# Kernel optimization log

Hardware: AMD Instinct MI355X
Metric: run time of the kernel (lower is better)

Reference implementation:

```python
import jax, jax.numpy as jnp
import numpy as np

B, IC, N = 32, 1, 64
KN, KS, PAD = 128, 65, 16
R, LAT = 8, 32
LEAK = 0.01
THETA_PRIOR = float(np.pi)
HW = N + 2 * PAD - KS + 1  # 32
OFFSETS = np.array([0, np.pi/4, np.pi/2, 3*np.pi/4, np.pi, -3*np.pi/4, -np.pi/2, -np.pi/4], dtype=np.float32)


def rotate_filters(w, n_rot):
    """Bilinear rotation of [O,I,k,k] filters for n_rot angles, matching
    F.affine_grid/F.grid_sample with align_corners=False, zero padding.
    Returns [O*n_rot, I, k, k] (rotation-major within each O block)."""
    O, I, k, _ = w.shape
    thetas = (2.0 * jnp.pi / n_rot) * jnp.arange(n_rot, dtype=jnp.float32)
    coords = (2.0 * jnp.arange(k, dtype=jnp.float32) + 1.0) / k - 1.0  # normalized, align_corners=False
    yy, xx = jnp.meshgrid(coords, coords, indexing='ij')  # [k,k]
    cos = jnp.cos(thetas)[:, None, None]
    sin = jnp.sin(thetas)[:, None, None]
    xs = cos * xx + sin * yy   # [R,k,k] sample x (normalized)
    ys = -sin * xx + cos * yy  # [R,k,k] sample y
    px = ((xs + 1.0) * k - 1.0) * 0.5  # pixel coords
    py = ((ys + 1.0) * k - 1.0) * 0.5
    x0 = jnp.floor(px); y0 = jnp.floor(py)
    wx = px - x0; wy = py - y0

    def gather(yi, xi):
        valid = (yi >= 0) & (yi < k) & (xi >= 0) & (xi < k)
        yc = jnp.clip(yi, 0, k - 1).astype(jnp.int32)
        xc = jnp.clip(xi, 0, k - 1).astype(jnp.int32)
        v = w[:, :, yc, xc]  # [O,I,R,k,k]
        return v * valid.astype(w.dtype)

    out = (gather(y0, x0) * (1 - wy) * (1 - wx)
           + gather(y0, x0 + 1) * (1 - wy) * wx
           + gather(y0 + 1, x0) * wy * (1 - wx)
           + gather(y0 + 1, x0 + 1) * wy * wx)  # [O,I,R,k,k]
    return jnp.transpose(out, (0, 2, 1, 3, 4)).reshape(O * n_rot, I, k, k)


def conv1x1(h, w, b):
    # h: [B,C,R,H,W], w: [O,C], b: [O] -- Conv3d with 1x1x1 kernel
    return jnp.einsum('bcrhw,oc->borhw', h, w) + b[None, :, None, None, None]


def _forward(x, w1, b1, w2, b2, wa, ba, wr, br, wz, bz, gumbel):
    tw = rotate_filters(w1[:, :, 0], R)  # [KN*R, IC, KS, KS]
    y = jax.lax.conv_general_dilated(
        x, tw, window_strides=(1, 1), padding=[(PAD, PAD), (PAD, PAD)],
        dimension_numbers=('NCHW', 'OIHW', 'NCHW'))
    Bn = y.shape[0]
    y = y.reshape(Bn, KN, R, HW, HW) + b1[None, :, None, None, None]
    xa = jax.nn.leaky_relu(y, LEAK)
    h = jax.nn.leaky_relu(conv1x1(xa, w2, b2), LEAK)
    attn = conv1x1(h, wa, ba)[:, 0]  # [B,R,H,W]
    offsets = jnp.asarray(OFFSETS)
    # Normal(0, theta_prior).log_prob(offsets)
    p_r = (-0.5 * (offsets / THETA_PRIOR) ** 2
           - jnp.log(THETA_PRIOR) - 0.5 * jnp.log(2.0 * jnp.pi))[:, None, None]  # [R,1,1]
    attn = attn + p_r  # broadcast over batch
    flat = attn.reshape(Bn, -1)
    q_t_r = jax.nn.log_softmax(flat, axis=1).reshape(attn.shape)
    a_sampled = jax.nn.softmax(flat + gumbel.reshape(Bn, -1), axis=-1).reshape(Bn, R, HW, HW)
    z = conv1x1(h, wz, bz)      # [B,2*LAT,R,H,W]
    theta = conv1x1(h, wr, br)  # [B,2,R,H,W]
    theta_mu = theta[:, 0] + offsets[None, :, None, None]
    theta = jnp.stack((theta_mu, theta[:, 1]), axis=1)
    return attn, q_t_r, p_r, a_sampled, offsets, theta, z


def setup_inputs():
    key = jax.random.key(0)
    ks = jax.random.split(key, 12)
    stdv1 = 1.0 / np.sqrt(IC * KS * KS)
    stdv2 = 1.0 / np.sqrt(KN)
    def unif(k, shape, a):
        return jax.random.uniform(k, shape, jnp.float32, -a, a)
    u = jax.random.uniform(ks[11], (B, R, HW, HW), jnp.float32, 1e-6, 1.0 - 1e-6)
    gumbel = -jnp.log(-jnp.log(u))
    return {
        'x': jax.random.normal(ks[0], (B, IC, N, N), jnp.float32),
        'w1': unif(ks[1], (KN, IC, 1, KS, KS), stdv1),
        'b1': unif(ks[2], (KN,), stdv1),
        'w2': unif(ks[3], (KN, KN), stdv2),
        'b2': unif(ks[4], (KN,), stdv2),
        'wa': unif(ks[5], (1, KN), stdv2),
        'ba': unif(ks[6], (1,), stdv2),
        'wr': unif(ks[7], (2, KN), stdv2),
        'br': unif(ks[8], (2,), stdv2),
        'wz': unif(ks[9], (2 * LAT, KN), stdv2),
        'bz': unif(ks[10], (2 * LAT,), stdv2),
        'gumbel': gumbel,
    }


def reference(x, w1, b1, w2, b2, wa, ba, wr, br, wz, bz, gumbel):
    return _forward(x, w1, b1, w2, b2, wa, ba, wr, br, wz, bz, gumbel)
```

## Files before the change

### kernel.cpp

```cpp
#include <hip/hip_runtime.h>
#include <hip/hip_bf16.h>

typedef unsigned int u32;
typedef unsigned short u16;

#define KYP 72
#define KPAD 4736
#define NK   74

#define OUT_ATTN 0
#define OUT_QTR  262144
#define OUT_PR   524288
#define OUT_AS   524296
#define OUT_OFF  786440
#define OUT_TH   786448
#define OUT_Z    1310736

typedef __attribute__((ext_vector_type(8))) short bf16x8;
typedef __attribute__((ext_vector_type(4))) float f32x4;

__device__ const float OFFS[8] = {
  0.0f,
  0.78539816339744830961f,
  1.57079632679489661923f,
  2.35619449019234492885f,
  3.14159265358979323846f,
 -2.35619449019234492885f,
 -1.57079632679489661923f,
 -0.78539816339744830961f
};

__device__ __forceinline__ float leaky_(float v){ return v >= 0.0f ? v : 0.01f*v; }

__device__ __forceinline__ u16 f2bf(float f){
  u32 x = __float_as_uint(f);
  u32 r = (x + 0x7FFFu + ((x >> 16) & 1u)) >> 16;
  return (u16)r;
}

__device__ __forceinline__ void gload_lds16(const void* g, void* l){
  __builtin_amdgcn_global_load_lds((const __attribute__((address_space(1))) u32*)g,
                                   (__attribute__((address_space(3))) u32*)l, 16, 0, 0);
}

#define BARRIER() { asm volatile("" ::: "memory"); __builtin_amdgcn_s_barrier(); asm volatile("" ::: "memory"); }
#define WAITV(N)  asm volatile("s_waitcnt vmcnt(" #N ")" ::: "memory")
#define LGK0()    { asm volatile("s_waitcnt lgkmcnt(0)" ::: "memory"); __builtin_amdgcn_sched_barrier(0); }
#define SCHEDB()  __builtin_amdgcn_sched_barrier(0)

__global__ __launch_bounds__(256) void xshift_kernel(const float* __restrict__ x, u16* __restrict__ xsh){
  int t = blockIdx.x*256 + threadIdx.x;
  if (t >= 393216) return;
  int c8  = t & 15;
  int u   = t >> 4;
  int row = u % 96;
  int v   = u / 96;
  int b   = v & 31;
  int s   = v >> 5;
  int iy = row - 16;
  u16 h[8];
#pragma unroll
  for (int j = 0; j < 8; ++j){
    int ix = c8*8 + j + s - 16;
    float val = 0.0f;
    if (iy >= 0 && iy < 64 && ix >= 0 && ix < 64) val = x[(b*64 + iy)*64 + ix];
    h[j] = f2bf(val);
  }
  uint4 pk;
  pk.x = (u32)h[0] | ((u32)h[1] << 16);
  pk.y = (u32)h[2] | ((u32)h[3] << 16);
  pk.z = (u32)h[4] | ((u32)h[5] << 16);
  pk.w = (u32)h[6] | ((u32)h[7] << 16);
  ((uint4*)xsh)[t] = pk;
}

__global__ __launch_bounds__(256) void rotate_kernel(const float* __restrict__ w1, u16* __restrict__ twb){
  __shared__ float wsh[4225];
  int n = blockIdx.x;
  int kn = n & 127, rot = n >> 7;
  for (int i = threadIdx.x; i < 4225; i += 256) wsh[i] = w1[kn*4225 + i];
  __syncthreads();
  float th  = 0.78539816339744830961f * (float)rot;
  float cth = cosf(th), sth = sinf(th);
  for (int t = threadIdx.x; t < KPAD; t += 256){
    int ky = t / KYP, kx = t - ky*KYP;
    u16 out = 0;
    if (ky < 65 && kx < 65){
      float yy = (2.0f*(float)ky + 1.0f)/65.0f - 1.0f;
      float xx = (2.0f*(float)kx + 1.0f)/65.0f - 1.0f;
      float xs  =  cth*xx + sth*yy;
      float ysv = -sth*xx + cth*yy;
      float px = ((xs  + 1.0f)*65.0f - 1.0f)*0.5f;
      float py = ((ysv + 1.0f)*65.0f - 1.0f)*0.5f;
      float x0 = floorf(px), y0 = floorf(py);
      float wx = px - x0, wy = py - y0;
      auto samp = [&](float yf, float xf)->float{
        bool valid = (yf >= 0.0f) && (yf < 65.0f) && (xf >= 0.0f) && (xf < 65.0f);
        int yc = (int)fminf(fmaxf(yf, 0.0f), 64.0f);
        int xc = (int)fminf(fmaxf(xf, 0.0f), 64.0f);
        return valid ? wsh[yc*65 + xc] : 0.0f;
      };
      float val = samp(y0,      x0     )*(1.0f-wy)*(1.0f-wx)
                + samp(y0,      x0+1.0f)*(1.0f-wy)*wx
                + samp(y0+1.0f, x0     )*wy*(1.0f-wx)
                + samp(y0+1.0f, x0+1.0f)*wy*wx;
      out = f2bf(val);
    }
    twb[(size_t)n*KPAD + t] = out;
  }
}

__global__ __launch_bounds__(512, 2) void gemm_kernel(const u16* __restrict__ xsh,
                                                      const u16* __restrict__ twb,
                                                      u16* __restrict__ ys){
  __shared__ u16 AsB[2*16384];
  __shared__ u16 BsB[2*16384];

  const int bid  = blockIdx.x;
  const int nblk = bid & 3, mblk = bid >> 2;
  const int t    = threadIdx.x;
  const int lane = t & 63, w = t >> 6;
  const int wr   = w >> 2, wn = w & 3;
  const int hi8  = (lane >> 4) << 3;

  const int sr  = t >> 3;
  const int j0e = (t & 7) * 8;
  const int jsw = j0e ^ ((sr & 7) << 3);
  const int bg  = mblk >> 4;
  const int ox2 = (mblk & 15) * 2;
  int aOff[4];
#pragma unroll
  for (int c = 0; c < 4; ++c){
    int i  = c*64 + sr;
    int ox = ox2 + (i >> 7);
    int s_ = ox & 7, colb = ox & ~7;
    int b_ = (bg << 2) + ((i & 127) >> 5);
    int oy = i & 31;
    aOff[c] = ((s_*32 + b_)*96 + oy)*128 + colb;
  }
  const u16* bPtr[4];
#pragma unroll
  for (int c = 0; c < 4; ++c){
    int nloc = c*64 + sr;
    bPtr[c] = twb + (size_t)(nblk*256 + nloc)*KPAD + jsw;
  }

  auto stageA4 = [&](int kt, u16* dstbase){
    int k = kt*64 + jsw;
    u32 ky = (u32)k / (u32)KYP;
    int kx0 = k - (int)ky*KYP;
    bool pad = (ky >= 65);
    int kofs = (int)ky*128 + kx0;
    const int ord[4] = {0, 2, 1, 3};
#pragma unroll
    for (int ii = 0; ii < 4; ++ii){
      int c = ord[ii];
      int gofs = pad ? 0 : (aOff[c] + kofs);
      gload_lds16(xsh + gofs, dstbase + c*4096 + w*512);
    }
  };
  auto stageB4 = [&](int kt, u16* dstbase){
    int ktc = (kt < NK) ? kt : (NK-1);
#pragma unroll
    for (int c = 0; c < 4; ++c)
      gload_lds16(bPtr[c] + ktc*64, dstbase + c*4096 + w*512);
  };

  f32x4 acc[8][4];
#pragma unroll
  for (int i = 0; i < 8; ++i)
#pragma unroll
    for (int j = 0; j < 4; ++j) acc[i][j] = (f32x4){0.f,0.f,0.f,0.f};
  bf16x8 amat[4][2], bmat[4][2];

  auto readA = [&](int mh, const char* Ab){
#pragma unroll
    for (int mj = 0; mj < 4; ++mj){
      int row = wr*128 + mh*64 + mj*16 + (lane & 15);
#pragma unroll
      for (int kk = 0; kk < 2; ++kk){
        int off = (row*128 + (kk*32 + hi8)*2) ^ ((row & 7) << 4);
        amat[mj][kk] = *(const bf16x8*)(Ab + off);
      }
    }
  };
  auto readB = [&](int nh, const char* Bb){
#pragma unroll
    for (int jn = 0; jn < 2; ++jn){
      int row = wn*64 + (nh*2 + jn)*16 + (lane & 15);
#pragma unroll
      for (int kk = 0; kk < 2; ++kk){
        int off = (row*128 + (kk*32 + hi8)*2) ^ ((row & 7) << 4);
        bmat[nh*2 + jn][kk] = *(const bf16x8*)(Bb + off);
      }
    }
  };
  auto mfma16 = [&](int MH, int NH){
    __builtin_amdgcn_s_setprio(1);
#pragma unroll
    for (int mj = 0; mj < 4; ++mj)
#pragma unroll
      for (int jn = 0; jn < 2; ++jn)
#pragma unroll
        for (int kk = 0; kk < 2; ++kk)
          acc[MH*4+mj][NH*2+jn] = __builtin_amdgcn_mfma_f32_16x16x32_bf16(
              amat[mj][kk], bmat[NH*2+jn][kk], acc[MH*4+mj][NH*2+jn], 0, 0, 0);
    __builtin_amdgcn_s_setprio(0);
  };

  u16* const A0 = AsB;
  u16* const B0 = BsB;
  u16* const A1 = AsB + 16384;
  u16* const B1 = BsB + 16384;

  stageB4(0, B0);
  stageA4(0, A0);
  WAITV(2);
  BARRIER();

  for (int kt = 0; kt < NK; ++kt){
    u16* Ab = (kt & 1) ? A1 : A0;
    u16* Bb = (kt & 1) ? B1 : B0;
    u16* An = (kt & 1) ? A0 : A1;
    u16* Bn = (kt & 1) ? B0 : B1;
    readA(0, (const char*)Ab); readB(0, (const char*)Bb);
    stageB4(kt+1, Bn);
    BARRIER();
    LGK0();
    mfma16(0, 0);
    SCHEDB();
    BARRIER();
    readB(1, (const char*)Bb);
    stageA4(kt+1, An);
    BARRIER();
    LGK0();
    mfma16(0, 1);
    SCHEDB();
    WAITV(8);
    BARRIER();
    readA(1, (const char*)Ab);
    BARRIER();
    LGK0();
    mfma16(1, 1);
    SCHEDB();
    BARRIER();
    mfma16(1, 0);
    SCHEDB();
    WAITV(2);
    BARRIER();
  }

  const int m_base = mblk*256 + wr*128;
  const int n_base = nblk*256 + wn*64;
  const int rsub = (lane >> 4) << 2;
  const int csub = lane & 15;
#pragma unroll
  for (int mf = 0; mf < 8; ++mf)
#pragma unroll
    for (int nf = 0; nf < 4; ++nf)
#pragma unroll
      for (int j = 0; j < 4; ++j){
        int m = m_base + mf*16 + rsub + j;
        int n = n_base + nf*16 + csub;
        ys[(size_t)m*1024 + n] = f2bf(acc[mf][nf][j]);
      }
}

__global__ __launch_bounds__(512) void mix_kernel(const u16* __restrict__ ys,
    const float* __restrict__ b1, const float* __restrict__ w2, const float* __restrict__ b2,
    const float* __restrict__ wa, const float* __restrict__ ba,
    const float* __restrict__ wr, const float* __restrict__ br,
    const float* __restrict__ wz, const float* __restrict__ bz,
    float* __restrict__ out){
  __shared__ __align__(16) u16 Ah[256*128];
  __shared__ __align__(16) u16 W2s[128*128];
  __shared__ __align__(16) u16 Wcs[80*128];
  __shared__ float b2s[128];
  __shared__ float bcs[80];

  const int blk = blockIdx.x;
  const int b   = blk >> 5, oy = blk & 31;
  const int t    = threadIdx.x;
  const int lane = t & 63;
  const int w    = t >> 6;

  {
    const int kn0 = (t & 15)*8;
    const int r_  = (t >> 4) & 7;
    float b1v[8];
#pragma unroll
    for (int j = 0; j < 8; ++j) b1v[j] = b1[kn0 + j];
#pragma unroll
    for (int i = 0; i < 8; ++i){
      int m_loc = 4*i + (t >> 7);
      int row_m = (((b >> 2)*32 + m_loc)*128) + (b & 3)*32 + oy;
      uint4 v = *(const uint4*)(ys + (size_t)row_m*1024 + r_*128 + kn0);
      u32 vv[4] = {v.x, v.y, v.z, v.w};
      u16 hh[8];
#pragma unroll
      for (int j = 0; j < 4; ++j){
        float lo = __uint_as_float(vv[j] << 16);
        float hi = __uint_as_float(vv[j] & 0xFFFF0000u);
        hh[2*j]   = f2bf(leaky_(lo + b1v[2*j]));
        hh[2*j+1] = f2bf(leaky_(hi + b1v[2*j+1]));
      }
      int Arow = r_*32 + m_loc;
      int off = (Arow*256 + kn0*2) ^ ((Arow & 7) << 4);
      uint4 pk;
      pk.x = (u32)hh[0] | ((u32)hh[1] << 16);
      pk.y = (u32)hh[2] | ((u32)hh[3] << 16);
      pk.z = (u32)hh[4] | ((u32)hh[5] << 16);
      pk.w = (u32)hh[6] | ((u32)hh[7] << 16);
      *(uint4*)((char*)Ah + off) = pk;
    }
  }
#pragma unroll
  for (int i = 0; i < 4; ++i){
    int ch = i*512 + t;
    int row = ch >> 4, kn0 = (ch & 15)*8;
    const float* src = w2 + row*128 + kn0;
    u16 hh[8];
#pragma unroll
    for (int j = 0; j < 8; ++j) hh[j] = f2bf(src[j]);
    int off = (row*256 + kn0*2) ^ ((row & 7) << 4);
    uint4 pk;
    pk.x = (u32)hh[0] | ((u32)hh[1] << 16);
    pk.y = (u32)hh[2] | ((u32)hh[3] << 16);
    pk.z = (u32)hh[4] | ((u32)hh[5] << 16);
    pk.w = (u32)hh[6] | ((u32)hh[7] << 16);
    *(uint4*)((char*)W2s + off) = pk;
  }
#pragma unroll
  for (int i = 0; i < 3; ++i){
    int ch = i*512 + t;
    if (ch < 1280){
      int row = ch >> 4, kn0 = (ch & 15)*8;
      const float* src = nullptr;
      if (row < 64)      src = wz + row*128 + kn0;
      else if (row == 64) src = wa + kn0;
      else if (row == 65) src = wr + kn0;
      else if (row == 66) src = wr + 128 + kn0;
      u16 hh[8];
#pragma unroll
      for (int j = 0; j < 8; ++j) hh[j] = src ? f2bf(src[j]) : (u16)0;
      int off = (row*256 + kn0*2) ^ ((row & 7) << 4);
      uint4 pk;
      pk.x = (u32)hh[0] | ((u32)hh[1] << 16);
      pk.y = (u32)hh[2] | ((u32)hh[3] << 16);
      pk.z = (u32)hh[4] | ((u32)hh[5] << 16);
      pk.w = (u32)hh[6] | ((u32)hh[7] << 16);
      *(uint4*)((char*)Wcs + off) = pk;
    }
  }
  if (t < 128) b2s[t] = b2[t];
  if (t < 80){
    float v = 0.0f;
    if (t < 64) v = bz[t];
    else if (t == 64) v = ba[0];
    else if (t == 65) v = br[0];
    else if (t == 66) v = br[1];
    bcs[t] = v;
  }
  __syncthreads();

  f32x4 acc1[2][8];
#pragma unroll
  for (int mf = 0; mf < 2; ++mf)
#pragma unroll
    for (int nf = 0; nf < 8; ++nf) acc1[mf][nf] = (f32x4){0.f,0.f,0.f,0.f};
#pragma unroll
  for (int kk = 0; kk < 128; kk += 32){
    int kb = (kk + ((lane >> 4) << 3))*2;
    bf16x8 a[2], bv[8];
#pragma unroll
    for (int mf = 0; mf < 2; ++mf){
      int row = w*32 + mf*16 + (lane & 15);
      int off = (row*256 + kb) ^ ((row & 7) << 4);
      a[mf] = *(const bf16x8*)((const char*)Ah + off);
    }
#pragma unroll
    for (int nf = 0; nf < 8; ++nf){
      int row = nf*16 + (lane & 15);
      int off = (row*256 + kb) ^ ((row & 7) << 4);
      bv[nf] = *(const bf16x8*)((const char*)W2s + off);
    }
#pragma unroll
    for (int mf = 0; mf < 2; ++mf)
#pragma unroll
      for (int nf = 0; nf < 8; ++nf)
        acc1[mf][nf] = __builtin_amdgcn_mfma_f32_16x16x32_bf16(a[mf], bv[nf], acc1[mf][nf], 0, 0, 0);
  }
  __syncthreads();

#pragma unroll
  for (int mf = 0; mf < 2; ++mf)
#pragma unroll
    for (int nf = 0; nf < 8; ++nf){
      int col = nf*16 + (lane & 15);
      float bb = b2s[col];
#pragma unroll
      for (int j = 0; j < 4; ++j){
        int row = w*32 + mf*16 + ((lane >> 4) << 2) + j;
        u16 hv = f2bf(leaky_(acc1[mf][nf][j] + bb));
        int off = (row*256 + col*2) ^ ((row & 7) << 4);
        *(u16*)((char*)Ah + off) = hv;
      }
    }
  __syncthreads();

  f32x4 acc2[2][5];
#pragma unroll
  for (int mf = 0; mf < 2; ++mf)
#pragma unroll
    for (int nf = 0; nf < 5; ++nf) acc2[mf][nf] = (f32x4){0.f,0.f,0.f,0.f};
#pragma unroll
  for (int kk = 0; kk < 128; kk += 32){
    int kb = (kk + ((lane >> 4) << 3))*2;
    bf16x8 a[2], bv[5];
#pragma unroll
    for (int mf = 0; mf < 2; ++mf){
      int row = w*32 + mf*16 + (lane & 15);
      int off = (row*256 + kb) ^ ((row & 7) << 4);
      a[mf] = *(const bf16x8*)((const char*)Ah + off);
    }
#pragma unroll
    for (int nf = 0; nf < 5; ++nf){
      int row = nf*16 + (lane & 15);
      int off = (row*256 + kb) ^ ((row & 7) << 4);
      bv[nf] = *(const bf16x8*)((const char*)Wcs + off);
    }
#pragma unroll
    for (int mf = 0; mf < 2; ++mf)
#pragma unroll
      for (int nf = 0; nf < 5; ++nf)
        acc2[mf][nf] = __builtin_amdgcn_mfma_f32_16x16x32_bf16(a[mf], bv[nf], acc2[mf][nf], 0, 0, 0);
  }

  const int r = w;
  float off_r = OFFS[r];
  float qn = off_r / 3.14159265358979323846f;
  float pr = -0.5f*qn*qn - 1.14472988584940017414f - 0.91893853320467274178f;
  const int pixb = oy*32;
#pragma unroll
  for (int mf = 0; mf < 2; ++mf)
#pragma unroll
    for (int nf = 0; nf < 5; ++nf){
      int c = nf*16 + (lane & 15);
#pragma unroll
      for (int j = 0; j < 4; ++j){
        int ox = mf*16 + ((lane >> 4) << 2) + j;
        float val = acc2[mf][nf][j];
        if (c < 64){
          out[OUT_Z + (size_t)b*524288 + (size_t)c*8192 + r*1024 + pixb + ox] = val + bcs[c];
        } else if (c == 64){
          out[OUT_ATTN + (size_t)(b*8 + r)*1024 + pixb + ox] = val + bcs[64] + pr;
        } else if (c == 65){
          out[OUT_TH + ((size_t)b*2)*8192 + r*1024 + pixb + ox] = val + bcs[65] + off_r;
        } else if (c == 66){
          out[OUT_TH + ((size_t)b*2 + 1)*8192 + r*1024 + pixb + ox] = val + bcs[66];
        }
      }
    }
}

__global__ __launch_bounds__(256) void softmax_kernel(const float* __restrict__ gumbel, float* __restrict__ out){
  __shared__ float a[8192];
  __shared__ float red[256];
  const int b = blockIdx.x, t = threadIdx.x;
  const float* attn = out + OUT_ATTN + (size_t)b*8192;
  float m = -3.0e38f;
  for (int i = t; i < 8192; i += 256){ float v = attn[i]; a[i] = v; m = fmaxf(m, v); }
  red[t] = m; __syncthreads();
#pragma unroll
  for (int s = 128; s > 0; s >>= 1){ if (t < s) red[t] = fmaxf(red[t], red[t+s]); __syncthreads(); }
  m = red[0]; __syncthreads();
  float s1 = 0.0f;
  for (int i = t; i < 8192; i += 256) s1 += expf(a[i] - m);
  red[t] = s1; __syncthreads();
#pragma unroll
  for (int s = 128; s > 0; s >>= 1){ if (t < s) red[t] += red[t+s]; __syncthreads(); }
  float lse = m + logf(red[0]);
  __syncthreads();
  float* q = out + OUT_QTR + (size_t)b*8192;
  for (int i = t; i < 8192; i += 256) q[i] = a[i] - lse;
  const float* g = gumbel + (size_t)b*8192;
  float m2 = -3.0e38f;
  for (int i = t; i < 8192; i += 256){ float v = a[i] + g[i]; a[i] = v; m2 = fmaxf(m2, v); }
  __syncthreads();
  red[t] = m2; __syncthreads();
#pragma unroll
  for (int s = 128; s > 0; s >>= 1){ if (t < s) red[t] = fmaxf(red[t], red[t+s]); __syncthreads(); }
  m2 = red[0]; __syncthreads();
  float s2 = 0.0f;
  for (int i = t; i < 8192; i += 256) s2 += expf(a[i] - m2);
  red[t] = s2; __syncthreads();
#pragma unroll
  for (int s = 128; s > 0; s >>= 1){ if (t < s) red[t] += red[t+s]; __syncthreads(); }
  float inv = 1.0f/red[0];
  float* as_ = out + OUT_AS + (size_t)b*8192;
  for (int i = t; i < 8192; i += 256) as_[i] = expf(a[i] - m2)*inv;
}

__global__ void tiny_kernel(float* __restrict__ out){
  int t = threadIdx.x;
  if (t < 8){
    float off = OFFS[t];
    out[OUT_OFF + t] = off;
    float qn = off / 3.14159265358979323846f;
    out[OUT_PR + t] = -0.5f*qn*qn - 1.14472988584940017414f - 0.91893853320467274178f;
  }
}

extern "C" void kernel_launch(void* const* d_in, const int* in_sizes, int n_in,
                              void* d_out, int out_size, void* d_ws, size_t ws_size,
                              hipStream_t stream){
  const float* x      = (const float*)d_in[0];
  const float* w1     = (const float*)d_in[1];
  const float* b1     = (const float*)d_in[2];
  const float* w2     = (const float*)d_in[3];
  const float* b2     = (const float*)d_in[4];
  const float* wa     = (const float*)d_in[5];
  const float* ba     = (const float*)d_in[6];
  const float* wr     = (const float*)d_in[7];
  const float* br     = (const float*)d_in[8];
  const float* wz     = (const float*)d_in[9];
  const float* bz     = (const float*)d_in[10];
  const float* gumbel = (const float*)d_in[11];
  float* out = (float*)d_out;

  u16* twb = (u16*)d_ws;
  u16* xsh = twb + (size_t)1024*KPAD;
  u16* ys  = xsh + (size_t)8*32*96*128;

  xshift_kernel <<<1536, 256, 0, stream>>>(x, xsh);
  rotate_kernel <<<1024, 256, 0, stream>>>(w1, twb);
  gemm_kernel   <<<512,  512, 0, stream>>>(xsh, twb, ys);
  mix_kernel    <<<1024, 512, 0, stream>>>(ys, b1, w2, b2, wa, ba, wr, br, wz, bz, out);
  softmax_kernel<<<32,   256, 0, stream>>>(gumbel, out);
  tiny_kernel   <<<1,    64,  0, stream>>>(out);
}
```

Before: 367.8 us.

## Strip intra-iteration barriers from GEMM main loop and use incremental A-tile indexing

Removes most of the workgroup barriers and sched_barriers inside the K loop, so each iteration keeps only one full vmcnt(0) wait and one barrier at its end. The per-iteration integer division used to compute the ky/kx position of the A tile is replaced by an incrementally updated counter. The intent is to cut synchronisation stalls and address arithmetic. In exchange, global-to-LDS loads are no longer overlapped across sub-phases because the loop waits for all of them each iteration, and the changed wave scheduling may hurt the ping-pong MFMA/load interleave.

```diff
diff --git a/kernel.cpp b/kernel.cpp
--- a/kernel.cpp
+++ b/kernel.cpp
@@ -46,7 +46,6 @@
 #define BARRIER() { asm volatile("" ::: "memory"); __builtin_amdgcn_s_barrier(); asm volatile("" ::: "memory"); }
 #define WAITV(N)  asm volatile("s_waitcnt vmcnt(" #N ")" ::: "memory")
 #define LGK0()    { asm volatile("s_waitcnt lgkmcnt(0)" ::: "memory"); __builtin_amdgcn_sched_barrier(0); }
-#define SCHEDB()  __builtin_amdgcn_sched_barrier(0)
 
 __global__ __launch_bounds__(256) void xshift_kernel(const float* __restrict__ x, u16* __restrict__ xsh){
   int t = blockIdx.x*256 + threadIdx.x;
@@ -145,16 +144,11 @@
     bPtr[c] = twb + (size_t)(nblk*256 + nloc)*KPAD + jsw;
   }
 
-  auto stageA4 = [&](int kt, u16* dstbase){
-    int k = kt*64 + jsw;
-    u32 ky = (u32)k / (u32)KYP;
-    int kx0 = k - (int)ky*KYP;
+  auto stageA4 = [&](int ky, int kx0, u16* dstbase){
     bool pad = (ky >= 65);
-    int kofs = (int)ky*128 + kx0;
-    const int ord[4] = {0, 2, 1, 3};
-#pragma unroll
-    for (int ii = 0; ii < 4; ++ii){
-      int c = ord[ii];
+    int kofs = ky*128 + kx0;
+#pragma unroll
+    for (int c = 0; c < 4; ++c){
       int gofs = pad ? 0 : (aOff[c] + kofs);
       gload_lds16(xsh + gofs, dstbase + c*4096 + w*512);
     }
@@ -214,8 +208,10 @@
   u16* const B1 = BsB + 16384;
 
   stageB4(0, B0);
-  stageA4(0, A0);
-  WAITV(2);
+  stageA4(0, jsw, A0);
+  int kyN = (64 + jsw >= KYP) ? 1 : 0;
+  int kxN = 64 + jsw - (kyN ? KYP : 0);
+  WAITV(0);
   BARRIER();
 
   for (int kt = 0; kt < NK; ++kt){
@@ -225,28 +221,18 @@
     u16* Bn = (kt & 1) ? B0 : B1;
     readA(0, (const char*)Ab); readB(0, (const char*)Bb);
     stageB4(kt+1, Bn);
-    BARRIER();
     LGK0();
     mfma16(0, 0);
-    SCHEDB();
-    BARRIER();
     readB(1, (const char*)Bb);
-    stageA4(kt+1, An);
-    BARRIER();
+    stageA4(kyN, kxN, An);
     LGK0();
     mfma16(0, 1);
-    SCHEDB();
-    WAITV(8);
-    BARRIER();
     readA(1, (const char*)Ab);
-    BARRIER();
     LGK0();
     mfma16(1, 1);
-    SCHEDB();
-    BARRIER();
     mfma16(1, 0);
-    SCHEDB();
-    WAITV(2);
+    kxN += 64; if (kxN >= KYP){ kxN -= KYP; ++kyN; }
+    WAITV(0);
     BARRIER();
   }
 
```

Result: faster. 350.7 us (-4.6%).
